# Kernel tuning notes

Hardware: AMD Instinct MI355X
Metric: run time of the kernel (lower is better)

Reference implementation:

```python
import jax, jax.numpy as jnp
import numpy as np

N = 2_000_000
FEAT = 83      # mat_feature_len
DIMF = 64      # dim_features
LAT = 32       # latent_dim
INIT_RANGE = 0.02
SHIFT_INIT = 0.001
EPS = 1e-12


def setup_inputs() -> dict:
    key = jax.random.key(0)
    ks = jax.random.split(key, 8)
    inputs = jax.random.normal(ks[0], (N, FEAT), dtype=jnp.float32)
    keep = jax.random.bernoulli(ks[1], 0.5, (N,))
    inputs = inputs * keep[:, None].astype(jnp.float32)
    shift = jnp.full((1,), SHIFT_INIT, dtype=jnp.float32)  # ZeroShift scalar
    W1 = jax.random.normal(ks[2], (FEAT, DIMF), dtype=jnp.float32) * INIT_RANGE
    b1 = jnp.zeros((DIMF,), dtype=jnp.float32)
    Wh0 = jax.random.normal(ks[3], (DIMF, LAT), dtype=jnp.float32) * INIT_RANGE
    bh0 = jnp.zeros((LAT,), dtype=jnp.float32)
    Wh1 = jax.random.normal(ks[4], (LAT, LAT), dtype=jnp.float32) * INIT_RANGE
    bh1 = jnp.zeros((LAT,), dtype=jnp.float32)
    return {"inputs": inputs, "shift": shift, "W1": W1, "b1": b1,
            "Wh0": Wh0, "bh0": bh0, "Wh1": Wh1, "bh1": bh1}


def reference(inputs, shift, W1, b1, Wh0, bh0, Wh1, bh1):
    # mask_zero: a material row is valid iff any feature is nonzero
    mask = jnp.any(inputs != 0, axis=-1)  # (N,)
    # Original gathers valid rows, runs MLP, scatters back (zeros elsewhere).
    # All ops are row-wise, so compute densely and zero masked rows — same math.
    x = inputs + shift                            # ZeroShift (scalar shift)
    x = jax.nn.relu(x @ W1 + b1)                  # dens_1 -> (N, DIMF)
    x = jax.nn.relu(x @ Wh0 + bh0)                # hidden 0 -> (N, LAT)
    x = jax.nn.relu(x @ Wh1 + bh1)                # hidden 1 -> (N, LAT)
    # UnifyVector: L2-normalize rows
    norm = jnp.sqrt(jnp.sum(x * x, axis=-1, keepdims=True))
    emb = x / jnp.maximum(norm, EPS)
    emb = emb * mask[:, None].astype(emb.dtype)   # scatter_nd equivalent
    return (emb, emb, emb)
```

## Files before the change

kernel.cpp:

```cpp
#include <hip/hip_runtime.h>

#define FEAT 83
#define DIMF 64
#define LAT  32
#define THREADS 256
#define RPB  128

typedef __attribute__((ext_vector_type(8))) short bf16x8;
typedef __attribute__((ext_vector_type(4))) float f32x4;
typedef __attribute__((ext_vector_type(4))) unsigned u32x4;

#define WT1H 0
#define WT1L 6144
#define WT2H 12288
#define WT2L 14336
#define WT3H 16384
#define WT3L 17408
#define WS_SHORTS 18432

#define WOFF 21248
#define SM_SHORTS 39936

__device__ __forceinline__ short f2b(float f) {
    unsigned u = __float_as_uint(f);
    u += 0x7fffu + ((u >> 16) & 1u);
    return (short)(u >> 16);
}
__device__ __forceinline__ float b2f(short h) {
    return __uint_as_float(((unsigned)(unsigned short)h) << 16);
}

__global__ void prep_weights(const float* __restrict__ W1,
                             const float* __restrict__ Wh0,
                             const float* __restrict__ Wh1,
                             short* __restrict__ ws)
{
    const int stride = gridDim.x * blockDim.x;
    const int tid = blockIdx.x * blockDim.x + threadIdx.x;
    for (int idx = tid; idx < 64 * 96; idx += stride) {
        int c = idx / 96, k = idx - c * 96;
        float w = (k < FEAT) ? W1[k * 64 + c] : 0.f;
        short hi = f2b(w);
        ws[WT1H + idx] = hi;
        ws[WT1L + idx] = f2b(w - b2f(hi));
    }
    for (int idx = tid; idx < 32 * 64; idx += stride) {
        int c = idx >> 6, k = idx & 63;
        float w = Wh0[k * 32 + c];
        short hi = f2b(w);
        ws[WT2H + idx] = hi;
        ws[WT2L + idx] = f2b(w - b2f(hi));
    }
    for (int idx = tid; idx < 32 * 32; idx += stride) {
        int c = idx >> 5, k = idx & 31;
        float w = Wh1[k * 32 + c];
        short hi = f2b(w);
        ws[WT3H + idx] = hi;
        ws[WT3L + idx] = f2b(w - b2f(hi));
    }
}

__device__ __forceinline__ void unpack8(const unsigned* p, bf16x8& hi, bf16x8& lo) {
    union { bf16x8 v; unsigned u[4]; } H, L;
    #pragma unroll
    for (int d = 0; d < 4; ++d) {
        H.u[d] = __builtin_amdgcn_perm(p[2 * d + 1], p[2 * d], 0x07060302u);
        L.u[d] = __builtin_amdgcn_perm(p[2 * d + 1], p[2 * d], 0x05040100u);
    }
    hi = H.v; lo = L.v;
}

__global__ __launch_bounds__(THREADS, 2)
void material_encoder_kernel(const float* __restrict__ inp,
                             const float* __restrict__ shiftp,
                             const short* __restrict__ ws,
                             const float* __restrict__ b1,
                             const float* __restrict__ bh0,
                             const float* __restrict__ bh1,
                             float* __restrict__ out,
                             int nrows)
{
    __shared__ __align__(16) short sm[SM_SHORTS];
    float* xt     = (float*)sm;
    unsigned* scr = (unsigned*)((char*)sm + (threadIdx.x >> 6) * 10624);
    float* maskf  = (float*)((char*)sm + 79360);

    const int t    = threadIdx.x;
    const int lane = t & 63;
    const int wv   = t >> 6;
    const int lr   = lane & 15;
    const int lq   = (lane >> 4) & 3;

    f32x4 xreg[11];
    {
        const f32x4* __restrict__ src4 =
            (const f32x4*)(inp + (long long)blockIdx.x * (RPB * FEAT));
        #pragma unroll
        for (int it = 0; it < 11; ++it) {
            const int idx = it * THREADS + t;
            if (idx < (RPB * FEAT / 4)) xreg[it] = src4[idx];
        }
    }
    f32x4 wreg[9];
    {
        const f32x4* __restrict__ wsrc = (const f32x4*)ws;
        #pragma unroll
        for (int it = 0; it < 9; ++it) wreg[it] = wsrc[it * THREADS + t];
    }

    float bias1[4], bias2[2], bias3[2];
    #pragma unroll
    for (int n = 0; n < 4; ++n) bias1[n] = b1[lr + 16 * n];
    #pragma unroll
    for (int n = 0; n < 2; ++n) { bias2[n] = bh0[lr + 16 * n]; bias3[n] = bh1[lr + 16 * n]; }
    const float sh = shiftp[0];
    const int Rw = blockIdx.x * RPB + wv * 32;

    {
        f32x4* xdst = (f32x4*)sm;
        #pragma unroll
        for (int it = 0; it < 11; ++it) {
            const int idx = it * THREADS + t;
            if (idx < (RPB * FEAT / 4)) xdst[idx] = xreg[it];
        }
        f32x4* wdst = (f32x4*)(sm + WOFF);
        #pragma unroll
        for (int it = 0; it < 9; ++it) wdst[it * THREADS + t] = wreg[it];
    }
    __syncthreads();

    bf16x8 a1h[2][3], a1l[2][3];
    float nzm[2];
    #pragma unroll
    for (int m = 0; m < 2; ++m) {
        const float* __restrict__ xr = xt + (wv * 32 + 16 * m + lr) * FEAT;
        float nz = 0.f;
        #pragma unroll
        for (int s = 0; s < 3; ++s) {
            const int k0 = 32 * s + 8 * lq;
            bf16x8 fh, fl;
            #pragma unroll
            for (int i = 0; i < 8; ++i) {
                int kk = k0 + i;
                kk = (kk < FEAT) ? kk : (FEAT - 1);
                const float x = xr[kk];
                nz = fmaxf(nz, fabsf(x));
                const float xs = x + sh;
                const unsigned u = __float_as_uint(xs);
                fh[i] = (short)(u >> 16);
                fl[i] = f2b(xs - __uint_as_float(u & 0xffff0000u));
            }
            a1h[m][s] = fh;
            a1l[m][s] = fl;
        }
        nzm[m] = nz;
    }
    #pragma unroll
    for (int m = 0; m < 2; ++m) {
        nzm[m] = fmaxf(nzm[m], __shfl_xor(nzm[m], 16));
        nzm[m] = fmaxf(nzm[m], __shfl_xor(nzm[m], 32));
    }
    if (lq == 0) {
        maskf[wv * 32 + lr]      = nzm[0];
        maskf[wv * 32 + 16 + lr] = nzm[1];
    }

    f32x4 acc[2][4];
    #pragma unroll
    for (int m = 0; m < 2; ++m)
        #pragma unroll
        for (int n = 0; n < 4; ++n)
            acc[m][n] = (f32x4){bias1[n], bias1[n], bias1[n], bias1[n]};

    #pragma unroll
    for (int s = 0; s < 3; ++s)
        #pragma unroll
        for (int n = 0; n < 4; ++n) {
            bf16x8 bh = *(const bf16x8*)&sm[WOFF + WT1H + (lr + 16 * n) * 96 + 32 * s + 8 * lq];
            bf16x8 bl = *(const bf16x8*)&sm[WOFF + WT1L + (lr + 16 * n) * 96 + 32 * s + 8 * lq];
            #pragma unroll
            for (int m = 0; m < 2; ++m) {
                acc[m][n] = __builtin_amdgcn_mfma_f32_16x16x32_bf16(a1h[m][s], bh, acc[m][n], 0, 0, 0);
                acc[m][n] = __builtin_amdgcn_mfma_f32_16x16x32_bf16(a1l[m][s], bh, acc[m][n], 0, 0, 0);
                acc[m][n] = __builtin_amdgcn_mfma_f32_16x16x32_bf16(a1h[m][s], bl, acc[m][n], 0, 0, 0);
            }
        }

    f32x4 acc2[2][2];
    #pragma unroll
    for (int m = 0; m < 2; ++m)
        #pragma unroll
        for (int n = 0; n < 2; ++n)
            acc2[m][n] = (f32x4){bias2[n], bias2[n], bias2[n], bias2[n]};

    #pragma unroll
    for (int s = 0; s < 2; ++s) {
        #pragma unroll
        for (int m = 0; m < 2; ++m)
            #pragma unroll
            for (int np = 0; np < 2; ++np)
                #pragma unroll
                for (int r = 0; r < 4; ++r) {
                    const float hv = fmaxf(acc[m][2 * s + np][r], 0.f);
                    const unsigned u = __float_as_uint(hv);
                    const unsigned hiu = u & 0xffff0000u;
                    const unsigned lo16 =
                        (unsigned short)f2b(hv - __uint_as_float(hiu));
                    scr[(16 * m + 4 * lq + r) * 32 + lr + 16 * np] = hiu | lo16;
                }
        bf16x8 a2h[2], a2l[2];
        #pragma unroll
        for (int m = 0; m < 2; ++m) {
            unsigned p[8];
            *(u32x4*)&p[0] = *(const u32x4*)&scr[(lr + 16 * m) * 32 + 8 * lq];
            *(u32x4*)&p[4] = *(const u32x4*)&scr[(lr + 16 * m) * 32 + 8 * lq + 4];
            unpack8(p, a2h[m], a2l[m]);
        }
        #pragma unroll
        for (int n = 0; n < 2; ++n) {
            bf16x8 bh = *(const bf16x8*)&sm[WOFF + WT2H + (lr + 16 * n) * 64 + 32 * s + 8 * lq];
            bf16x8 bl = *(const bf16x8*)&sm[WOFF + WT2L + (lr + 16 * n) * 64 + 32 * s + 8 * lq];
            #pragma unroll
            for (int m = 0; m < 2; ++m) {
                acc2[m][n] = __builtin_amdgcn_mfma_f32_16x16x32_bf16(a2h[m], bh, acc2[m][n], 0, 0, 0);
                acc2[m][n] = __builtin_amdgcn_mfma_f32_16x16x32_bf16(a2l[m], bh, acc2[m][n], 0, 0, 0);
                acc2[m][n] = __builtin_amdgcn_mfma_f32_16x16x32_bf16(a2h[m], bl, acc2[m][n], 0, 0, 0);
            }
        }
    }

    f32x4 acc3[2][2];
    #pragma unroll
    for (int m = 0; m < 2; ++m)
        #pragma unroll
        for (int n = 0; n < 2; ++n)
            acc3[m][n] = (f32x4){bias3[n], bias3[n], bias3[n], bias3[n]};

    #pragma unroll
    for (int m = 0; m < 2; ++m)
        #pragma unroll
        for (int n = 0; n < 2; ++n)
            #pragma unroll
            for (int r = 0; r < 4; ++r) {
                const float gv = fmaxf(acc2[m][n][r], 0.f);
                const unsigned u = __float_as_uint(gv);
                const unsigned hiu = u & 0xffff0000u;
                const unsigned lo16 =
                    (unsigned short)f2b(gv - __uint_as_float(hiu));
                scr[(16 * m + 4 * lq + r) * 32 + lr + 16 * n] = hiu | lo16;
            }
    {
        bf16x8 a3h[2], a3l[2];
        #pragma unroll
        for (int m = 0; m < 2; ++m) {
            unsigned p[8];
            *(u32x4*)&p[0] = *(const u32x4*)&scr[(lr + 16 * m) * 32 + 8 * lq];
            *(u32x4*)&p[4] = *(const u32x4*)&scr[(lr + 16 * m) * 32 + 8 * lq + 4];
            unpack8(p, a3h[m], a3l[m]);
        }
        #pragma unroll
        for (int n = 0; n < 2; ++n) {
            bf16x8 bh = *(const bf16x8*)&sm[WOFF + WT3H + (lr + 16 * n) * 32 + 8 * lq];
            bf16x8 bl = *(const bf16x8*)&sm[WOFF + WT3L + (lr + 16 * n) * 32 + 8 * lq];
            #pragma unroll
            for (int m = 0; m < 2; ++m) {
                acc3[m][n] = __builtin_amdgcn_mfma_f32_16x16x32_bf16(a3h[m], bh, acc3[m][n], 0, 0, 0);
                acc3[m][n] = __builtin_amdgcn_mfma_f32_16x16x32_bf16(a3l[m], bh, acc3[m][n], 0, 0, 0);
                acc3[m][n] = __builtin_amdgcn_mfma_f32_16x16x32_bf16(a3h[m], bl, acc3[m][n], 0, 0, 0);
            }
        }
    }

    float er[2][2][4];
    float ssq[2][4];
    #pragma unroll
    for (int m = 0; m < 2; ++m)
        #pragma unroll
        for (int r = 0; r < 4; ++r) ssq[m][r] = 0.f;
    #pragma unroll
    for (int m = 0; m < 2; ++m)
        #pragma unroll
        for (int n = 0; n < 2; ++n)
            #pragma unroll
            for (int r = 0; r < 4; ++r) {
                float e = fmaxf(acc3[m][n][r], 0.f);
                er[m][n][r] = e;
                ssq[m][r] = fmaf(e, e, ssq[m][r]);
            }
    #pragma unroll
    for (int msk = 1; msk <= 8; msk <<= 1)
        #pragma unroll
        for (int m = 0; m < 2; ++m)
            #pragma unroll
            for (int r = 0; r < 4; ++r)
                ssq[m][r] += __shfl_xor(ssq[m][r], msk);

    const float* maskp = maskf + wv * 32;
    f32x4 mk[2];
    mk[0] = *(const f32x4*)&maskp[4 * lq];
    mk[1] = *(const f32x4*)&maskp[16 + 4 * lq];

    float sc[2][4];
    #pragma unroll
    for (int m = 0; m < 2; ++m)
        #pragma unroll
        for (int r = 0; r < 4; ++r)
            sc[m][r] = (mk[m][r] != 0.f) ? rsqrtf(fmaxf(ssq[m][r], 1e-24f)) : 0.f;

    const int osz = nrows * LAT;
    float* __restrict__ ob = out + (long long)Rw * LAT;
    #pragma unroll
    for (int m = 0; m < 2; ++m)
        #pragma unroll
        for (int r = 0; r < 4; ++r) {
            const int ro = (16 * m + 4 * lq + r) * LAT;
            #pragma unroll
            for (int n = 0; n < 2; ++n) {
                const float vv = er[m][n][r] * sc[m][r];
                const int cc = ro + lr + 16 * n;
                ob[cc]           = vv;
                ob[osz + cc]     = vv;
                ob[2 * osz + cc] = vv;
            }
        }
}

extern "C" void kernel_launch(void* const* d_in, const int* in_sizes, int n_in,
                              void* d_out, int out_size, void* d_ws, size_t ws_size,
                              hipStream_t stream) {
    const float* inp    = (const float*)d_in[0];
    const float* shiftp = (const float*)d_in[1];
    const float* W1     = (const float*)d_in[2];
    const float* b1     = (const float*)d_in[3];
    const float* Wh0    = (const float*)d_in[4];
    const float* bh0    = (const float*)d_in[5];
    const float* Wh1    = (const float*)d_in[6];
    const float* bh1    = (const float*)d_in[7];
    float* out = (float*)d_out;
    short* ws  = (short*)d_ws;

    const int nrows = in_sizes[0] / FEAT;
    const int blocks = nrows / RPB;

    prep_weights<<<dim3(24), dim3(THREADS), 0, stream>>>(W1, Wh0, Wh1, ws);
    material_encoder_kernel<<<dim3(blocks), dim3(THREADS), 0, stream>>>(
        inp, shiftp, ws, b1, bh0, bh1, out, nrows);
}
```

Baseline: 283.7 us.

## Alias input staging and weight LDS regions to fit three blocks per CU

Each wave now stages only its own 32 input rows in a private LDS slice. The weight copy is written later into the same memory, after all waves have built their bf16 A fragments from the inputs, with barriers around it. This shrinks shared memory from about 80KB to about 54KB, and launch bounds is raised to 3 blocks per CU to raise occupancy and latency hiding for this memory-bound kernel. In exchange it adds an extra barrier, and the weight LDS write now sits in the critical path after the input conversion.

```diff
diff --git a/kernel.cpp b/kernel.cpp
--- a/kernel.cpp
+++ b/kernel.cpp
@@ -18,8 +18,7 @@
 #define WT3L 17408
 #define WS_SHORTS 18432
 
-#define WOFF 21248
-#define SM_SHORTS 39936
+#define SM_SHORTS 26880
 
 __device__ __forceinline__ short f2b(float f) {
     unsigned u = __float_as_uint(f);
@@ -70,7 +69,7 @@
     hi = H.v; lo = L.v;
 }
 
-__global__ __launch_bounds__(THREADS, 2)
+__global__ __launch_bounds__(THREADS, 3)
 void material_encoder_kernel(const float* __restrict__ inp,
                              const float* __restrict__ shiftp,
                              const short* __restrict__ ws,
@@ -81,9 +80,8 @@
                              int nrows)
 {
     __shared__ __align__(16) short sm[SM_SHORTS];
-    float* xt     = (float*)sm;
-    unsigned* scr = (unsigned*)((char*)sm + (threadIdx.x >> 6) * 10624);
-    float* maskf  = (float*)((char*)sm + 79360);
+    unsigned* scr = (unsigned*)((char*)sm + 36864) + (threadIdx.x >> 6) * 1024;
+    float* maskf  = (float*)((char*)sm + 53248);
 
     const int t    = threadIdx.x;
     const int lane = t & 63;
@@ -91,21 +89,27 @@
     const int lr   = lane & 15;
     const int lq   = (lane >> 4) & 3;
 
+    float* xw = (float*)((char*)sm + wv * 10624);
+
     f32x4 xreg[11];
     {
-        const f32x4* __restrict__ src4 =
-            (const f32x4*)(inp + (long long)blockIdx.x * (RPB * FEAT));
-        #pragma unroll
-        for (int it = 0; it < 11; ++it) {
-            const int idx = it * THREADS + t;
-            if (idx < (RPB * FEAT / 4)) xreg[it] = src4[idx];
-        }
+        const f32x4* __restrict__ src4 = (const f32x4*)
+            (inp + (long long)blockIdx.x * (RPB * FEAT) + wv * (32 * FEAT));
+        #pragma unroll
+        for (int r = 0; r < 10; ++r) xreg[r] = src4[r * 64 + lane];
+        if (lane < 24) xreg[10] = src4[640 + lane];
     }
     f32x4 wreg[9];
     {
         const f32x4* __restrict__ wsrc = (const f32x4*)ws;
         #pragma unroll
         for (int it = 0; it < 9; ++it) wreg[it] = wsrc[it * THREADS + t];
+    }
+    {
+        f32x4* xdst = (f32x4*)xw;
+        #pragma unroll
+        for (int r = 0; r < 10; ++r) xdst[r * 64 + lane] = xreg[r];
+        if (lane < 24) xdst[640 + lane] = xreg[10];
     }
 
     float bias1[4], bias2[2], bias3[2];
@@ -116,24 +120,11 @@
     const float sh = shiftp[0];
     const int Rw = blockIdx.x * RPB + wv * 32;
 
-    {
-        f32x4* xdst = (f32x4*)sm;
-        #pragma unroll
-        for (int it = 0; it < 11; ++it) {
-            const int idx = it * THREADS + t;
-            if (idx < (RPB * FEAT / 4)) xdst[idx] = xreg[it];
-        }
-        f32x4* wdst = (f32x4*)(sm + WOFF);
-        #pragma unroll
-        for (int it = 0; it < 9; ++it) wdst[it * THREADS + t] = wreg[it];
-    }
-    __syncthreads();
-
     bf16x8 a1h[2][3], a1l[2][3];
     float nzm[2];
     #pragma unroll
     for (int m = 0; m < 2; ++m) {
-        const float* __restrict__ xr = xt + (wv * 32 + 16 * m + lr) * FEAT;
+        const float* __restrict__ xr = xw + (16 * m + lr) * FEAT;
         float nz = 0.f;
         #pragma unroll
         for (int s = 0; s < 3; ++s) {
@@ -165,6 +156,15 @@
         maskf[wv * 32 + 16 + lr] = nzm[1];
     }
 
+    __syncthreads();
+
+    {
+        f32x4* wdst = (f32x4*)sm;
+        #pragma unroll
+        for (int it = 0; it < 9; ++it) wdst[it * THREADS + t] = wreg[it];
+    }
+    __syncthreads();
+
     f32x4 acc[2][4];
     #pragma unroll
     for (int m = 0; m < 2; ++m)
@@ -176,8 +176,8 @@
     for (int s = 0; s < 3; ++s)
         #pragma unroll
         for (int n = 0; n < 4; ++n) {
-            bf16x8 bh = *(const bf16x8*)&sm[WOFF + WT1H + (lr + 16 * n) * 96 + 32 * s + 8 * lq];
-            bf16x8 bl = *(const bf16x8*)&sm[WOFF + WT1L + (lr + 16 * n) * 96 + 32 * s + 8 * lq];
+            bf16x8 bh = *(const bf16x8*)&sm[WT1H + (lr + 16 * n) * 96 + 32 * s + 8 * lq];
+            bf16x8 bl = *(const bf16x8*)&sm[WT1L + (lr + 16 * n) * 96 + 32 * s + 8 * lq];
             #pragma unroll
             for (int m = 0; m < 2; ++m) {
                 acc[m][n] = __builtin_amdgcn_mfma_f32_16x16x32_bf16(a1h[m][s], bh, acc[m][n], 0, 0, 0);
@@ -218,8 +218,8 @@
         }
         #pragma unroll
         for (int n = 0; n < 2; ++n) {
-            bf16x8 bh = *(const bf16x8*)&sm[WOFF + WT2H + (lr + 16 * n) * 64 + 32 * s + 8 * lq];
-            bf16x8 bl = *(const bf16x8*)&sm[WOFF + WT2L + (lr + 16 * n) * 64 + 32 * s + 8 * lq];
+            bf16x8 bh = *(const bf16x8*)&sm[WT2H + (lr + 16 * n) * 64 + 32 * s + 8 * lq];
+            bf16x8 bl = *(const bf16x8*)&sm[WT2L + (lr + 16 * n) * 64 + 32 * s + 8 * lq];
             #pragma unroll
             for (int m = 0; m < 2; ++m) {
                 acc2[m][n] = __builtin_amdgcn_mfma_f32_16x16x32_bf16(a2h[m], bh, acc2[m][n], 0, 0, 0);
@@ -260,8 +260,8 @@
         }
         #pragma unroll
         for (int n = 0; n < 2; ++n) {
-            bf16x8 bh = *(const bf16x8*)&sm[WOFF + WT3H + (lr + 16 * n) * 32 + 8 * lq];
-            bf16x8 bl = *(const bf16x8*)&sm[WOFF + WT3L + (lr + 16 * n) * 32 + 8 * lq];
+            bf16x8 bh = *(const bf16x8*)&sm[WT3H + (lr + 16 * n) * 32 + 8 * lq];
+            bf16x8 bl = *(const bf16x8*)&sm[WT3L + (lr + 16 * n) * 32 + 8 * lq];
             #pragma unroll
             for (int m = 0; m < 2; ++m) {
                 acc3[m][n] = __builtin_amdgcn_mfma_f32_16x16x32_bf16(a3h[m], bh, acc3[m][n], 0, 0, 0);
```

Measured after the change: 265.6 us. -6.4%, faster.
